# Kernel optimization log

Hardware: AMD Instinct MI355X
Metric: run time of the kernel (lower is better)

Reference implementation:

```python
import jax, jax.numpy as jnp
from jax import lax
import numpy as np

NSTEP, NGRID, MU = 365, 4000, 8
STAIND = NSTEP - 1          # time index providing static parameters
TDLST = [1, 2, 3, 4, 5]     # 1-based indices of dynamic parameters
HBV_LO = jnp.array([0.0, 1.0, 0.005, 0.005, 0.0, 0.0, 0.005, 0.005, 0.0, 0.0, 0.0], jnp.float32)
HBV_HI = jnp.array([1.0, 2000.0, 0.995, 0.995, 1.0, 7.0, 0.995, 0.995, 1.0, 1.0, 1.0], jnp.float32)
SMIN = 1e-4                 # clamp floor for states
CAPMIN = 0.005 / 4          # floor for derived capacities

# ---- MARRMoT-style flux helpers (all elementwise) ----

def split_1(p1, In):
    return p1 * In

def soilmoisture_1(S1, S1max, S2, S2max):
    mask = (S1 / S1max < S2 / S2max).astype(S1.dtype)
    return (S2 * S1max - S1 * S2max) / (S1max + S2max) * mask

def soilmoisture_2(S1, S1max, S2, S2max, S3, S3max):
    # water rebalance to equal relative storage (3 stores); flux drawn from S2
    mask = (S1 / S1max < (S2 + S3) / (S2max + S3max)).astype(S1.dtype)
    return (S2 * S1max - S1 * S2max) / (S1max + S2max + S3max) * mask

def evap_7(S, Smax, Ep, dt):
    return jnp.minimum(S / Smax * Ep, S / dt)

def evap_1(S, Ep, dt):
    return jnp.minimum(Ep, S / dt)

def saturation_1(In, S, Smax):
    return In * (S >= Smax).astype(In.dtype)

def interflow_5(p1, S):
    return p1 * S

def baseflow_1(p1, S):
    return p1 * S

def percolation_4(pbase, zperc, rexp, deficit, defmax, S, Smax, dt):
    pc = pbase * (1.0 + zperc * (deficit / defmax) ** (1.0 + rexp)) * S / Smax
    return jnp.maximum(0.0, jnp.minimum(pc, S / dt))

def deficit_dist(S1, S1max, S2, S2max):
    d1 = jnp.maximum(0.0, 1.0 - S1 / S1max)
    d2 = jnp.maximum(0.0, 1.0 - S2 / S2max)
    tot = d1 + d2
    return jnp.where(tot > 0, d1 / jnp.where(tot > 0, tot, 1.0), S1max / (S1max + S2max))


def _forward(x, parameters):
    Nstep, Ngrid = x.shape[0], x.shape[1]
    mu = parameters.shape[3]
    P_ = x[:, :, 0]   # [Nstep, Ngrid]
    Ep_ = x[:, :, 2]  # [Nstep, Ngrid]

    # scale raw [0,1] params to physical ranges
    parT = HBV_LO[None, None, :, None] + parameters * (HBV_HI - HBV_LO)[None, None, :, None]
    parsta = parT[STAIND]  # [Ngrid, 11, mu] static params
    dyn = np.zeros(11, dtype=bool)
    for ix in TDLST:
        dyn[ix - 1] = True
    dyn = jnp.asarray(dyn)
    # dydrop=0 -> dynamic params always used on tdlst slots, static elsewhere
    parhbv = jnp.where(dyn[None, None, :, None], parT, parsta[None])  # [Nstep,Ngrid,11,mu]

    S0 = jnp.full((Ngrid, mu), 0.001, x.dtype)

    def step(carry, inp):
        S1, S2, S3, S4, S5 = carry
        Pt, Ept, par = inp            # par: [Ngrid, 11, mu]
        P = Pt[:, None]               # [Ngrid, 1] broadcasts against [Ngrid, mu]
        Ep = Ept[:, None]
        pctim, smax, f1, f2, kuz, rexp, f3, f4, pfree, klzp, klzs = [par[:, i, :] for i in range(11)]

        uztwm = f1 * smax
        uzfwm = jnp.maximum(CAPMIN, f2 * (smax - uztwm))
        lztwm = jnp.maximum(CAPMIN, f3 * (smax - uztwm - uzfwm))
        lzfwpm = jnp.maximum(CAPMIN, f4 * (smax - uztwm - uzfwm - lztwm))
        lzfwsm = jnp.maximum(CAPMIN, (1.0 - f4) * (smax - uztwm - uzfwm - lztwm))
        pbase = lzfwpm * klzp + lzfwsm * klzs
        denom = lzfwsm * klzs + lzfwpm * klzp
        zperc = jnp.minimum(1e5, (lztwm + lzfwsm * (1.0 - klzs)) / denom + lzfwpm * (1.0 - klzp) / denom)
        dt = 1.0

        flux_qdir = split_1(pctim, P)
        flux_peff = split_1(1.0 - pctim, P)
        flux_ru = soilmoisture_1(S1, uztwm, S2, uzfwm)
        flux_euztw = evap_7(S1, uztwm, Ep, dt)
        flux_twexu = saturation_1(flux_peff, S1, uztwm)
        flux_qsur = saturation_1(flux_twexu, S2, uzfwm)
        flux_qint = interflow_5(kuz, S2)
        flux_euzfw = evap_1(S2, jnp.maximum(0.0, Ep - flux_euztw), dt)
        deficit = (jnp.maximum(1e-8, lztwm - S3) + jnp.maximum(1e-8, lzfwpm - S4)
                   + jnp.maximum(1e-8, lzfwsm - S5))
        defmax = jnp.maximum(1e-8, lztwm + lzfwpm + lzfwsm)
        flux_pc = percolation_4(pbase, zperc, rexp, deficit, defmax, S2, uzfwm, dt)
        flux_pctw = split_1(1.0 - pfree, flux_pc)
        flux_elztw = evap_7(S3, lztwm, jnp.maximum(0.0, Ep - flux_euztw - flux_euzfw), dt)
        flux_twexl = saturation_1(flux_pctw, S3, lztwm)
        fp = deficit_dist(S4, lzfwpm, S5, lzfwsm)
        fs = deficit_dist(S5, lzfwsm, S4, lzfwpm)
        flux_twexlp = split_1(fp, flux_twexl)
        flux_twexls = split_1(fs, flux_twexl)
        flux_pcfwp = split_1(pfree * fp, flux_pc)
        flux_pcfws = split_1(pfree * fs, flux_pc)
        flux_rlp = soilmoisture_2(S3, lztwm, S4, lzfwpm, S5, lzfwsm)
        flux_rls = soilmoisture_2(S3, lztwm, S5, lzfwsm, S4, lzfwpm)
        flux_qbfp = baseflow_1(klzp, S4)
        flux_qbfs = baseflow_1(klzs, S5)

        nS1 = jnp.maximum(S1 + flux_peff + flux_ru - flux_euztw - flux_twexu, SMIN)
        nS2 = jnp.maximum(S2 + flux_twexu - flux_euzfw - flux_qsur - flux_qint - flux_ru - flux_pc, SMIN)
        nS3 = jnp.maximum(S3 + flux_pctw + flux_rlp + flux_rls - flux_elztw - flux_twexl, SMIN)
        nS4 = jnp.maximum(S4 + flux_twexlp + flux_pcfwp - flux_rlp - flux_qbfp, SMIN)
        nS5 = jnp.maximum(S5 + flux_twexls + flux_pcfws - flux_rls - flux_qbfs, SMIN)

        qsim = flux_qdir + flux_qsur + flux_qint + flux_qbfp + flux_qbfs
        et = flux_euztw + flux_euzfw + flux_elztw
        return (nS1, nS2, nS3, nS4, nS5), (qsim, et)

    _, (Qsimmu, ETmu) = lax.scan(step, (S0, S0, S0, S0, S0), (P_, Ep_, parhbv))
    Qs = Qsimmu.mean(-1, keepdims=True)      # muwts=None -> mean over components
    ETave = ETmu.mean(-1, keepdims=True)
    return jnp.concatenate([Qs, ETave], axis=-1)  # [Nstep, Ngrid, 2]


def setup_inputs() -> dict:
    key = jax.random.key(0)
    k1, k2 = jax.random.split(key)
    x = jax.random.uniform(k1, (NSTEP, NGRID, 3), dtype=jnp.float32)
    parameters = jax.random.uniform(k2, (NSTEP, NGRID, 11, MU), dtype=jnp.float32)
    return {"x": x, "parameters": parameters}


def reference(x, parameters):
    return _forward(x, parameters)
```

## Files before the change

kernel.cpp:

```cpp
#include <hip/hip_runtime.h>
#include <stdint.h>

#define NSTEP 365
#define NGRID 4000
#define CAPMIN 0.00125f
#define SMINV 0.0001f
#define PSTR_DW (NGRID * 88)
#define XSTR_DW (NGRID * 3)

#define RAW_REG  1728
#define X_OFF    1600
#define DER_BASE 6912
#define DER_SLOT 768
#define DER_REG  3840
#define STG_BASE 14592
#define STG_REG  640

typedef __attribute__((address_space(3))) uint32_t lds_u32_t;
typedef __attribute__((address_space(1))) uint32_t glb_u32_t;

__device__ __forceinline__ void dma4(const float* g, float* l) {
    __builtin_amdgcn_global_load_lds((const glb_u32_t*)(const void*)g,
                                     (lds_u32_t*)(void*)l, 4, 0, 0);
}

__device__ __forceinline__ float frcp(float x) { return __builtin_amdgcn_rcpf(x); }
__device__ __forceinline__ float fexp2(float x) { return __builtin_amdgcn_exp2f(x); }
__device__ __forceinline__ float flog2(float x) { return __builtin_amdgcn_logf(x); }

#define RDS(j)                                                               \
    const float  c0_##j = rreg[(j) * 320 + lane];                            \
    const float  kz_##j = rreg[(j) * 320 + 256 + lane];                      \
    const float  Pp_##j = xreg[(j) * 24 + gl3];                              \
    const float  Ee_##j = xreg[(j) * 24 + gl3 + 2];                          \
    const float2 dA_##j = dreg[(j) * 384 + lane];                            \
    const float2 dB_##j = dreg[(j) * 384 + 64 + lane];                       \
    const float2 dC_##j = dreg[(j) * 384 + 128 + lane];                      \
    const float2 dD_##j = dreg[(j) * 384 + 192 + lane];                      \
    const float2 dE_##j = dreg[(j) * 384 + 256 + lane];                      \
    const float2 dF_##j = dreg[(j) * 384 + 320 + lane];

#define STEP(j) do {                                                         \
    const float uztwm = dA_##j.x, uzfwm = dA_##j.y;                          \
    const float inv_uztwm = dB_##j.x, inv_uzfwm = dB_##j.y;                  \
    const float inv_uzsum = dC_##j.x, lztwm = dC_##j.y;                      \
    const float inv_lztwm = dD_##j.x, pbase = dD_##j.y;                      \
    const float lzfwpm = dE_##j.x, lzfwsm = dE_##j.y;                        \
    const float pz = dF_##j.x, inv_defmax = dF_##j.y;                        \
    const float Ep = Ee_##j, kuz = kz_##j;                                   \
    const float qdir = c0_##j * Pp_##j;                                      \
    const float peff = Pp_##j - qdir;                                        \
    const float rud  = S2 * uztwm - S1 * uzfwm;                              \
    const float ru   = (rud > 0.0f) ? rud * inv_uzsum : 0.0f;                \
    const float euztw = fminf(S1 * inv_uztwm * Ep, S1);                      \
    const float twexu = (S1 >= uztwm) ? peff : 0.0f;                         \
    const float qsur  = (S2 >= uzfwm) ? twexu : 0.0f;                        \
    const float qint  = kuz * S2;                                            \
    const float euzfw = fminf(fmaxf(0.0f, Ep - euztw), S2);                  \
    const float deficit = fmaxf(1e-8f, lztwm - S3)                           \
                        + fmaxf(1e-8f, lzfwpm - S4)                          \
                        + fmaxf(1e-8f, lzfwsm - S5);                         \
    const float powterm = fexp2(e1 * flog2(deficit * inv_defmax));           \
    const float pc = fminf((pbase + pz * powterm) * (S2 * inv_uzfwm), S2);   \
    const float pctw  = (1.0f - pfree) * pc;                                 \
    const float elztw = fminf(S3 * inv_lztwm                                 \
                              * fmaxf(0.0f, Ep - euztw - euzfw), S3);        \
    const float twexl = (S3 >= lztwm) ? pctw : 0.0f;                         \
    const float aa  = fmaxf(0.0f, lzfwpm - S4) * lzfwsm;                     \
    const float bb  = fmaxf(0.0f, lzfwsm - S5) * lzfwpm;                     \
    const float den = aa + bb;                                               \
    const float pm  = lzfwpm + lzfwsm;                                       \
    const float fp  = ((den > 0.0f) ? aa : lzfwpm)                           \
                    * frcp((den > 0.0f) ? den : pm);                         \
    const float fs  = 1.0f - fp;                                             \
    const float twexlp = fp * twexl;                                         \
    const float twexls = fs * twexl;                                         \
    const float pcfwp  = pfree * fp * pc;                                    \
    const float pcfws  = pfree * fs * pc;                                    \
    const bool rlm = S3 * pm < (S4 + S5) * lztwm;                            \
    const float rlp = rlm ? (S4 * lztwm - S3 * lzfwpm) * inv_defmax : 0.0f;  \
    const float rls = rlm ? (S5 * lztwm - S3 * lzfwsm) * inv_defmax : 0.0f;  \
    const float qbfp = klzp * S4;                                            \
    const float qbfs = klzs * S5;                                            \
    S1 = fmaxf(S1 + peff + ru - euztw - twexu, SMINV);                       \
    S2 = fmaxf(S2 + twexu - euzfw - qsur - qint - ru - pc, SMINV);           \
    S3 = fmaxf(S3 + pctw + rlp + rls - elztw - twexl, SMINV);                \
    S4 = fmaxf(S4 + twexlp + pcfwp - rlp - qbfp, SMINV);                     \
    S5 = fmaxf(S5 + twexls + pcfws - rls - qbfs, SMINV);                     \
    stq[(j) * 64 + lane] = qdir + qsur + qint + qbfp + qbfs;                 \
    stq[320 + (j) * 64 + lane] = euztw + euzfw + elztw;                      \
} while (0)

__global__ __launch_bounds__(192, 1) void sacsma_kernel(
    const float* __restrict__ x,
    const float* __restrict__ par,
    float* __restrict__ out)
{
    __shared__ __align__(16) float lds[15872];

    const int wave = threadIdx.x >> 6;
    const int lane = threadIdx.x & 63;
    const int g0   = blockIdx.x * 8;
    const int gl   = lane >> 3;
    const int mu   = lane & 7;
    const int g    = g0 + gl;

    if (wave == 0) {
        __builtin_amdgcn_s_setprio(0);
        const float* pp = par + (size_t)g * 88 + mu;
        const int tA = lane / 24;
        const int rA = lane - 24 * tA;
        int idxB = lane + 64;
        int tB = idxB / 24;
        int rB = idxB - 24 * tB;
        if (tB > 4) { tB = 4; rB = idxB - 120; }
        const float* pxA = x + (size_t)tA * XSTR_DW + g0 * 3 + rA;
        const float* pxB = x + (size_t)tB * XSTR_DW + g0 * 3 + rB;

        #define ISSUE_BATCH(b) do {                                          \
            float* reg_ = lds + ((b) & 3) * RAW_REG;                         \
            const int tb_ = 5 * (b);                                         \
            _Pragma("unroll")                                                \
            for (int j = 0; j < 5; ++j) {                                    \
                const float* pj_ = pp + (size_t)(tb_ + j) * PSTR_DW;         \
                float* dst_ = reg_ + j * 320;                                \
                dma4(pj_,      dst_);                                        \
                dma4(pj_ + 8,  dst_ + 64);                                   \
                dma4(pj_ + 16, dst_ + 128);                                  \
                dma4(pj_ + 24, dst_ + 192);                                  \
                dma4(pj_ + 32, dst_ + 256);                                  \
            }                                                                \
            dma4(pxA + (size_t)tb_ * XSTR_DW, reg_ + X_OFF);                 \
            dma4(pxB + (size_t)tb_ * XSTR_DW, reg_ + X_OFF + 64);            \
        } while (0)

        #define REDUCE_STORE(b) do {                                         \
            if (lane < 40) {                                                 \
                const float* stg_ = lds + STG_BASE + ((b) & 1) * STG_REG;    \
                const int s_  = lane >> 3;                                   \
                const int gg_ = lane & 7;                                    \
                const float4 qa = *(const float4*)&stg_[s_ * 64 + gg_ * 8];  \
                const float4 qb = *(const float4*)&stg_[s_ * 64 + gg_ * 8 + 4];\
                const float4 ea = *(const float4*)&stg_[320 + s_ * 64 + gg_ * 8];\
                const float4 eb = *(const float4*)&stg_[320 + s_ * 64 + gg_ * 8 + 4];\
                const float qsum = ((qa.x + qa.y) + (qa.z + qa.w))           \
                                 + ((qb.x + qb.y) + (qb.z + qb.w));          \
                const float esum = ((ea.x + ea.y) + (ea.z + ea.w))           \
                                 + ((eb.x + eb.y) + (eb.z + eb.w));          \
                float2 o = make_float2(qsum * 0.125f, esum * 0.125f);        \
                *reinterpret_cast<float2*>(                                   \
                    out + ((size_t)(5 * (b) + s_) * NGRID + g0 + gg_) * 2) = o;\
            }                                                                \
        } while (0)

        ISSUE_BATCH(0);

        for (int ip = 0; ip < 75; ++ip) {
            if (ip >= 3)
                REDUCE_STORE(ip - 3);
            if (ip <= 71) {
                ISSUE_BATCH(ip + 1);
                asm volatile("s_waitcnt vmcnt(27)" ::: "memory");
            } else {
                asm volatile("s_waitcnt vmcnt(0)" ::: "memory");
            }
            asm volatile("s_barrier" ::: "memory");
        }
        REDUCE_STORE(72);
    } else if (wave == 1) {
        __builtin_amdgcn_s_setprio(1);
        const float* ps = par + ((size_t)(NSTEP - 1) * NGRID + g) * 88 + mu;
        const float f3   = 0.005f + ps[6 * 8] * 0.99f;
        const float f4   = 0.005f + ps[7 * 8] * 0.99f;
        const float klzp = ps[9 * 8];
        const float klzs = ps[10 * 8];

        for (int i = 0; i < 75; ++i) {
            if (i >= 1 && i <= 73) {
                const int b = i - 1;
                const float* rreg = lds + (b & 3) * RAW_REG;
                float* dregf = lds + DER_BASE + (b & 1) * DER_REG;
                #pragma unroll
                for (int j = 0; j < 5; ++j) {
                    const float* rb = rreg + j * 320;
                    float2* db = reinterpret_cast<float2*>(dregf + j * DER_SLOT);

                    const float c1 = rb[64 + lane];
                    const float c2 = rb[128 + lane];
                    const float c3 = rb[192 + lane];

                    const float smaxv = 1.0f + c1 * 1999.0f;
                    const float f1 = 0.005f + c2 * 0.99f;
                    const float f2 = 0.005f + c3 * 0.99f;
                    const float uztwm = f1 * smaxv;
                    float rem = smaxv - uztwm;
                    const float uzfwm = fmaxf(CAPMIN, f2 * rem);
                    rem -= uzfwm;
                    const float lztwm = fmaxf(CAPMIN, f3 * rem);
                    rem -= lztwm;
                    const float lzfwpm = fmaxf(CAPMIN, f4 * rem);
                    const float lzfwsm = fmaxf(CAPMIN, (1.0f - f4) * rem);
                    const float pbase = lzfwpm * klzp + lzfwsm * klzs;
                    const float pz = fminf(lztwm + lzfwsm * (1.0f - klzs)
                                           + lzfwpm * (1.0f - klzp),
                                           100000.0f * pbase);
                    const float inv_uztwm = frcp(uztwm);
                    const float inv_uzfwm = frcp(uzfwm);
                    const float inv_lztwm = frcp(lztwm);
                    const float inv_uzsum = frcp(uztwm + uzfwm);
                    const float inv_defmax = frcp(lztwm + lzfwpm + lzfwsm);

                    db[0 * 64 + lane] = make_float2(uztwm, uzfwm);
                    db[1 * 64 + lane] = make_float2(inv_uztwm, inv_uzfwm);
                    db[2 * 64 + lane] = make_float2(inv_uzsum, lztwm);
                    db[3 * 64 + lane] = make_float2(inv_lztwm, pbase);
                    db[4 * 64 + lane] = make_float2(lzfwpm, lzfwsm);
                    db[5 * 64 + lane] = make_float2(pz, inv_defmax);
                }
                asm volatile("s_waitcnt lgkmcnt(0)" ::: "memory");
            }
            asm volatile("s_barrier" ::: "memory");
        }
    } else {
        __builtin_amdgcn_s_setprio(2);
        const float* ps = par + ((size_t)(NSTEP - 1) * NGRID + g) * 88 + mu;
        const float e1    = 1.0f + ps[5 * 8] * 7.0f;
        const float pfree = ps[8 * 8];
        const float klzp  = ps[9 * 8];
        const float klzs  = ps[10 * 8];

        float S1 = 0.001f, S2 = 0.001f, S3 = 0.001f, S4 = 0.001f, S5 = 0.001f;
        const int gl3 = gl * 3;

        for (int i = 0; i < 75; ++i) {
            if (i >= 2) {
                const int b = i - 2;
                const float* rreg = lds + (b & 3) * RAW_REG;
                const float* xreg = rreg + X_OFF;
                const float2* dreg = reinterpret_cast<const float2*>(
                    lds + DER_BASE + (b & 1) * DER_REG);
                float* stq = lds + STG_BASE + (b & 1) * STG_REG;

                RDS(0) RDS(1) RDS(2) RDS(3) RDS(4)
                STEP(0); STEP(1); STEP(2); STEP(3); STEP(4);

                asm volatile("s_waitcnt lgkmcnt(0)" ::: "memory");
            }
            asm volatile("s_barrier" ::: "memory");
        }
    }
}

extern "C" void kernel_launch(void* const* d_in, const int* in_sizes, int n_in,
                              void* d_out, int out_size, void* d_ws, size_t ws_size,
                              hipStream_t stream) {
    const float* x   = (const float*)d_in[0];
    const float* par = (const float*)d_in[1];
    float* out = (float*)d_out;

    sacsma_kernel<<<NGRID / 8, 192, 0, stream>>>(x, par, out);
}
```

Before: 128.2 us.

## Move per-step precompute and output reduction to the derive wave, shrink raw ring

Result: slower. 136.3 us (+6.3%).

```diff
diff --git a/kernel.cpp b/kernel.cpp
--- a/kernel.cpp
+++ b/kernel.cpp
@@ -10,10 +10,10 @@
 
 #define RAW_REG  1728
 #define X_OFF    1600
-#define DER_BASE 6912
-#define DER_SLOT 768
-#define DER_REG  3840
-#define STG_BASE 14592
+#define DER_BASE 5184
+#define DER_SLOT 896
+#define DER_REG  4480
+#define STG_BASE 14144
 #define STG_REG  640
 
 typedef __attribute__((address_space(3))) uint32_t lds_u32_t;
@@ -29,59 +29,54 @@
 __device__ __forceinline__ float flog2(float x) { return __builtin_amdgcn_logf(x); }
 
 #define RDS(j)                                                               \
-    const float  c0_##j = rreg[(j) * 320 + lane];                            \
-    const float  kz_##j = rreg[(j) * 320 + 256 + lane];                      \
-    const float  Pp_##j = xreg[(j) * 24 + gl3];                              \
-    const float  Ee_##j = xreg[(j) * 24 + gl3 + 2];                          \
-    const float2 dA_##j = dreg[(j) * 384 + lane];                            \
-    const float2 dB_##j = dreg[(j) * 384 + 64 + lane];                       \
-    const float2 dC_##j = dreg[(j) * 384 + 128 + lane];                      \
-    const float2 dD_##j = dreg[(j) * 384 + 192 + lane];                      \
-    const float2 dE_##j = dreg[(j) * 384 + 256 + lane];                      \
-    const float2 dF_##j = dreg[(j) * 384 + 320 + lane];
+    const float2 qp_##j = dreg[(j) * 448 + lane];            \
+    const float2 ek_##j = dreg[(j) * 448 +  64 + lane];      \
+    const float2 iu_##j = dreg[(j) * 448 + 128 + lane];     \
+    const float2 hl_##j = dreg[(j) * 448 + 192 + lane];     \
+    const float2 ip_##j = dreg[(j) * 448 + 256 + lane];     \
+    const float2 lz_##j = dreg[(j) * 448 + 320 + lane];     \
+    const float2 pz_##j = dreg[(j) * 448 + 384 + lane];
 
 #define STEP(j) do {                                                         \
-    const float uztwm = dA_##j.x, uzfwm = dA_##j.y;                          \
-    const float inv_uztwm = dB_##j.x, inv_uzfwm = dB_##j.y;                  \
-    const float inv_uzsum = dC_##j.x, lztwm = dC_##j.y;                      \
-    const float inv_lztwm = dD_##j.x, pbase = dD_##j.y;                      \
-    const float lzfwpm = dE_##j.x, lzfwsm = dE_##j.y;                        \
-    const float pz = dF_##j.x, inv_defmax = dF_##j.y;                        \
-    const float Ep = Ee_##j, kuz = kz_##j;                                   \
-    const float qdir = c0_##j * Pp_##j;                                      \
-    const float peff = Pp_##j - qdir;                                        \
-    const float rud  = S2 * uztwm - S1 * uzfwm;                              \
-    const float ru   = (rud > 0.0f) ? rud * inv_uzsum : 0.0f;                \
-    const float euztw = fminf(S1 * inv_uztwm * Ep, S1);                      \
-    const float twexu = (S1 >= uztwm) ? peff : 0.0f;                         \
-    const float qsur  = (S2 >= uzfwm) ? twexu : 0.0f;                        \
-    const float qint  = kuz * S2;                                            \
+    const float qdir = qp_##j.x, peff = qp_##j.y;                            \
+    const float Ep = ek_##j.x, kuz = ek_##j.y;                               \
+    const float inv_uztwm = iu_##j.x, inv_uzfwm = iu_##j.y;                  \
+    const float hmean = hl_##j.x, lztwm = hl_##j.y;                          \
+    const float inv_lztwm = ip_##j.x, pbase = ip_##j.y;                      \
+    const float lzfwpm = lz_##j.x, lzfwsm = lz_##j.y;                        \
+    const float pz = pz_##j.x, inv_defmax = pz_##j.y;                        \
+    const float r1 = S1 * inv_uztwm;                                         \
+    const float r2 = S2 * inv_uzfwm;                                         \
+    const float euztw = fminf(r1 * Ep, S1);                                  \
+    const float twexu = (r1 >= 1.0f) ? peff : 0.0f;                          \
+    const float qsur  = (r2 >= 1.0f) ? twexu : 0.0f;                         \
+    const float rd = r2 - r1;                                                \
+    const float ru = (rd > 0.0f) ? rd * hmean : 0.0f;                        \
+    const float qint = kuz * S2;                                             \
     const float euzfw = fminf(fmaxf(0.0f, Ep - euztw), S2);                  \
-    const float deficit = fmaxf(1e-8f, lztwm - S3)                           \
-                        + fmaxf(1e-8f, lzfwpm - S4)                          \
-                        + fmaxf(1e-8f, lzfwsm - S5);                         \
+    const float t3 = lztwm - S3, t4 = lzfwpm - S4, t5 = lzfwsm - S5;         \
+    const float deficit = fmaxf(1e-8f, t3) + fmaxf(1e-8f, t4)                \
+                        + fmaxf(1e-8f, t5);                                  \
     const float powterm = fexp2(e1 * flog2(deficit * inv_defmax));           \
-    const float pc = fminf((pbase + pz * powterm) * (S2 * inv_uzfwm), S2);   \
-    const float pctw  = (1.0f - pfree) * pc;                                 \
-    const float elztw = fminf(S3 * inv_lztwm                                 \
-                              * fmaxf(0.0f, Ep - euztw - euzfw), S3);        \
+    const float pc = fminf((pbase + pz * powterm) * r2, S2);                 \
+    const float pctw = pfree1m * pc;                                         \
+    const float ev3 = fmaxf(0.0f, Ep - euztw - euzfw);                       \
+    const float elztw = fminf(S3 * inv_lztwm * ev3, S3);                     \
     const float twexl = (S3 >= lztwm) ? pctw : 0.0f;                         \
-    const float aa  = fmaxf(0.0f, lzfwpm - S4) * lzfwsm;                     \
-    const float bb  = fmaxf(0.0f, lzfwsm - S5) * lzfwpm;                     \
+    const float aa = fmaxf(0.0f, t4) * lzfwsm;                               \
+    const float bb = fmaxf(0.0f, t5) * lzfwpm;                               \
     const float den = aa + bb;                                               \
-    const float pm  = lzfwpm + lzfwsm;                                       \
-    const float fp  = ((den > 0.0f) ? aa : lzfwpm)                           \
-                    * frcp((den > 0.0f) ? den : pm);                         \
-    const float fs  = 1.0f - fp;                                             \
-    const float twexlp = fp * twexl;                                         \
-    const float twexls = fs * twexl;                                         \
-    const float pcfwp  = pfree * fp * pc;                                    \
-    const float pcfws  = pfree * fs * pc;                                    \
+    const float pm = lzfwpm + lzfwsm;                                        \
+    const float fp = ((den > 0.0f) ? aa : lzfwpm)                            \
+                   * frcp((den > 0.0f) ? den : pm);                          \
+    const float fs = 1.0f - fp;                                              \
+    const float pcp = pfree * pc;                                            \
+    const float twexlp = fp * twexl, twexls = fs * twexl;                    \
+    const float pcfwp = fp * pcp, pcfws = fs * pcp;                          \
     const bool rlm = S3 * pm < (S4 + S5) * lztwm;                            \
     const float rlp = rlm ? (S4 * lztwm - S3 * lzfwpm) * inv_defmax : 0.0f;  \
     const float rls = rlm ? (S5 * lztwm - S3 * lzfwsm) * inv_defmax : 0.0f;  \
-    const float qbfp = klzp * S4;                                            \
-    const float qbfs = klzs * S5;                                            \
+    const float qbfp = klzp * S4, qbfs = klzs * S5;                          \
     S1 = fmaxf(S1 + peff + ru - euztw - twexu, SMINV);                       \
     S2 = fmaxf(S2 + twexu - euzfw - qsur - qint - ru - pc, SMINV);           \
     S3 = fmaxf(S3 + pctw + rlp + rls - elztw - twexl, SMINV);                \
@@ -96,7 +91,7 @@
     const float* __restrict__ par,
     float* __restrict__ out)
 {
-    __shared__ __align__(16) float lds[15872];
+    __shared__ __align__(16) float lds[15424];
 
     const int wave = threadIdx.x >> 6;
     const int lane = threadIdx.x & 63;
@@ -104,21 +99,19 @@
     const int gl   = lane >> 3;
     const int mu   = lane & 7;
     const int g    = g0 + gl;
+    const int gl3  = gl * 3;
 
     if (wave == 0) {
-        __builtin_amdgcn_s_setprio(0);
         const float* pp = par + (size_t)g * 88 + mu;
-        const int tA = lane / 24;
-        const int rA = lane - 24 * tA;
+        const int tA = lane / 24, rA = lane - 24 * tA;
         int idxB = lane + 64;
-        int tB = idxB / 24;
-        int rB = idxB - 24 * tB;
+        int tB = idxB / 24, rB = idxB - 24 * tB;
         if (tB > 4) { tB = 4; rB = idxB - 120; }
         const float* pxA = x + (size_t)tA * XSTR_DW + g0 * 3 + rA;
         const float* pxB = x + (size_t)tB * XSTR_DW + g0 * 3 + rB;
 
         #define ISSUE_BATCH(b) do {                                          \
-            float* reg_ = lds + ((b) & 3) * RAW_REG;                         \
+            float* reg_ = lds + ((b) % 3) * RAW_REG;                         \
             const int tb_ = 5 * (b);                                         \
             _Pragma("unroll")                                                \
             for (int j = 0; j < 5; ++j) {                                    \
@@ -134,60 +127,45 @@
             dma4(pxB + (size_t)tb_ * XSTR_DW, reg_ + X_OFF + 64);            \
         } while (0)
 
-        #define REDUCE_STORE(b) do {                                         \
-            if (lane < 40) {                                                 \
-                const float* stg_ = lds + STG_BASE + ((b) & 1) * STG_REG;    \
-                const int s_  = lane >> 3;                                   \
-                const int gg_ = lane & 7;                                    \
-                const float4 qa = *(const float4*)&stg_[s_ * 64 + gg_ * 8];  \
-                const float4 qb = *(const float4*)&stg_[s_ * 64 + gg_ * 8 + 4];\
-                const float4 ea = *(const float4*)&stg_[320 + s_ * 64 + gg_ * 8];\
-                const float4 eb = *(const float4*)&stg_[320 + s_ * 64 + gg_ * 8 + 4];\
-                const float qsum = ((qa.x + qa.y) + (qa.z + qa.w))           \
-                                 + ((qb.x + qb.y) + (qb.z + qb.w));          \
-                const float esum = ((ea.x + ea.y) + (ea.z + ea.w))           \
-                                 + ((eb.x + eb.y) + (eb.z + eb.w));          \
-                float2 o = make_float2(qsum * 0.125f, esum * 0.125f);        \
-                *reinterpret_cast<float2*>(                                   \
-                    out + ((size_t)(5 * (b) + s_) * NGRID + g0 + gg_) * 2) = o;\
-            }                                                                \
-        } while (0)
-
         ISSUE_BATCH(0);
 
-        for (int ip = 0; ip < 75; ++ip) {
-            if (ip >= 3)
-                REDUCE_STORE(ip - 3);
-            if (ip <= 71) {
-                ISSUE_BATCH(ip + 1);
+        for (int i = 0; i < 76; ++i) {
+            if (i <= 71) {
+                ISSUE_BATCH(i + 1);
                 asm volatile("s_waitcnt vmcnt(27)" ::: "memory");
             } else {
                 asm volatile("s_waitcnt vmcnt(0)" ::: "memory");
             }
             asm volatile("s_barrier" ::: "memory");
         }
-        REDUCE_STORE(72);
     } else if (wave == 1) {
-        __builtin_amdgcn_s_setprio(1);
         const float* ps = par + ((size_t)(NSTEP - 1) * NGRID + g) * 88 + mu;
         const float f3   = 0.005f + ps[6 * 8] * 0.99f;
         const float f4   = 0.005f + ps[7 * 8] * 0.99f;
         const float klzp = ps[9 * 8];
         const float klzs = ps[10 * 8];
-
-        for (int i = 0; i < 75; ++i) {
+        const float f4m  = 1.0f - f4;
+        const float k1p  = 1.0f - klzp;
+        const float k1s  = 1.0f - klzs;
+
+        for (int i = 0; i < 76; ++i) {
             if (i >= 1 && i <= 73) {
                 const int b = i - 1;
-                const float* rreg = lds + (b & 3) * RAW_REG;
+                const float* rreg = lds + (b % 3) * RAW_REG;
                 float* dregf = lds + DER_BASE + (b & 1) * DER_REG;
                 #pragma unroll
                 for (int j = 0; j < 5; ++j) {
                     const float* rb = rreg + j * 320;
+                    const float* xb = rreg + X_OFF + j * 24;
                     float2* db = reinterpret_cast<float2*>(dregf + j * DER_SLOT);
 
+                    const float c0 = rb[lane];
                     const float c1 = rb[64 + lane];
                     const float c2 = rb[128 + lane];
                     const float c3 = rb[192 + lane];
+                    const float c4 = rb[256 + lane];
+                    const float P  = xb[gl3];
+                    const float Ep = xb[gl3 + 2];
 
                     const float smaxv = 1.0f + c1 * 1999.0f;
                     const float f1 = 0.005f + c2 * 0.99f;
@@ -199,44 +177,62 @@
                     const float lztwm = fmaxf(CAPMIN, f3 * rem);
                     rem -= lztwm;
                     const float lzfwpm = fmaxf(CAPMIN, f4 * rem);
-                    const float lzfwsm = fmaxf(CAPMIN, (1.0f - f4) * rem);
+                    const float lzfwsm = fmaxf(CAPMIN, f4m * rem);
                     const float pbase = lzfwpm * klzp + lzfwsm * klzs;
-                    const float pz = fminf(lztwm + lzfwsm * (1.0f - klzs)
-                                           + lzfwpm * (1.0f - klzp),
-                                           100000.0f * pbase);
+                    const float pzv = fminf(lztwm + lzfwsm * k1s + lzfwpm * k1p,
+                                            100000.0f * pbase);
                     const float inv_uztwm = frcp(uztwm);
                     const float inv_uzfwm = frcp(uzfwm);
                     const float inv_lztwm = frcp(lztwm);
-                    const float inv_uzsum = frcp(uztwm + uzfwm);
+                    const float hmean = uztwm * uzfwm * frcp(uztwm + uzfwm);
                     const float inv_defmax = frcp(lztwm + lzfwpm + lzfwsm);
-
-                    db[0 * 64 + lane] = make_float2(uztwm, uzfwm);
-                    db[1 * 64 + lane] = make_float2(inv_uztwm, inv_uzfwm);
-                    db[2 * 64 + lane] = make_float2(inv_uzsum, lztwm);
-                    db[3 * 64 + lane] = make_float2(inv_lztwm, pbase);
-                    db[4 * 64 + lane] = make_float2(lzfwpm, lzfwsm);
-                    db[5 * 64 + lane] = make_float2(pz, inv_defmax);
+                    const float qdir = c0 * P;
+
+                    db[0 * 64 + lane] = make_float2(qdir, P - qdir);
+                    db[1 * 64 + lane] = make_float2(Ep, c4);
+                    db[2 * 64 + lane] = make_float2(inv_uztwm, inv_uzfwm);
+                    db[3 * 64 + lane] = make_float2(hmean, lztwm);
+                    db[4 * 64 + lane] = make_float2(inv_lztwm, pbase);
+                    db[5 * 64 + lane] = make_float2(lzfwpm, lzfwsm);
+                    db[6 * 64 + lane] = make_float2(pzv, inv_defmax);
                 }
-                asm volatile("s_waitcnt lgkmcnt(0)" ::: "memory");
-            }
+            }
+            if (i >= 3) {
+                const int b = i - 3;
+                if (lane < 40) {
+                    const float* stg = lds + STG_BASE + (b & 1) * STG_REG;
+                    const int s  = lane >> 3;
+                    const int gg = lane & 7;
+                    const float4 qa = *(const float4*)&stg[s * 64 + gg * 8];
+                    const float4 qb = *(const float4*)&stg[s * 64 + gg * 8 + 4];
+                    const float4 ea = *(const float4*)&stg[320 + s * 64 + gg * 8];
+                    const float4 eb = *(const float4*)&stg[320 + s * 64 + gg * 8 + 4];
+                    const float qsum = ((qa.x + qa.y) + (qa.z + qa.w))
+                                     + ((qb.x + qb.y) + (qb.z + qb.w));
+                    const float esum = ((ea.x + ea.y) + (ea.z + ea.w))
+                                     + ((eb.x + eb.y) + (eb.z + eb.w));
+                    float2 o = make_float2(qsum * 0.125f, esum * 0.125f);
+                    *reinterpret_cast<float2*>(
+                        out + ((size_t)(5 * b + s) * NGRID + g0 + gg) * 2) = o;
+                }
+            }
+            asm volatile("s_waitcnt lgkmcnt(0)" ::: "memory");
             asm volatile("s_barrier" ::: "memory");
         }
     } else {
-        __builtin_amdgcn_s_setprio(2);
+        __builtin_amdgcn_s_setprio(1);
         const float* ps = par + ((size_t)(NSTEP - 1) * NGRID + g) * 88 + mu;
         const float e1    = 1.0f + ps[5 * 8] * 7.0f;
         const float pfree = ps[8 * 8];
         const float klzp  = ps[9 * 8];
         const float klzs  = ps[10 * 8];
+        const float pfree1m = 1.0f - pfree;
 
         float S1 = 0.001f, S2 = 0.001f, S3 = 0.001f, S4 = 0.001f, S5 = 0.001f;
-        const int gl3 = gl * 3;
-
-        for (int i = 0; i < 75; ++i) {
-            if (i >= 2) {
+
+        for (int i = 0; i < 76; ++i) {
+            if (i >= 2 && i <= 74) {
                 const int b = i - 2;
-                const float* rreg = lds + (b & 3) * RAW_REG;
-                const float* xreg = rreg + X_OFF;
                 const float2* dreg = reinterpret_cast<const float2*>(
                     lds + DER_BASE + (b & 1) * DER_REG);
                 float* stq = lds + STG_BASE + (b & 1) * STG_REG;
```
